# Performance work log

Hardware: AMD Instinct MI355X
Metric: run time of the kernel (lower is better)

Reference implementation:

```python
import jax, jax.numpy as jnp
import numpy as np

B, N = 128, 1024

def setup_inputs() -> dict:
    key = jax.random.key(0)
    k1, k2 = jax.random.split(key)
    probs = jax.random.uniform(k1, (B, N), dtype=jnp.float32)
    co_matrix = jax.random.uniform(k2, (N, N), dtype=jnp.float32)
    return {"probs": probs, "co_matrix": co_matrix}

def reference(probs, co_matrix):
    # diff[b, i, j] = probs[b, j] - probs[b, i]
    diff = probs[:, None, :] - probs[:, :, None]          # [B, N, N]
    weighted = jnp.square(diff) * co_matrix[None, :, :]   # [B, N, N]
    eps = 1e-8
    n_pos = jnp.sum((co_matrix > 0).astype(jnp.float32))
    # sum over (i, j) of mean over batch
    loss = jnp.sum(jnp.mean(weighted, axis=0)) / (n_pos + eps)
    return loss
```

## Files before the change

### kernel.cpp

```cpp
#include <hip/hip_runtime.h>


#define B_DIM 128
#define N_DIM 1024
#define TILE  64

__global__ __launch_bounds__(512) void tile_kernel(const float* __restrict__ P,
                                                   const float* __restrict__ C,
                                                   double* __restrict__ psum,
                                                   unsigned* __restrict__ pcnt) {
    __shared__ float Pi[B_DIM][TILE];
    __shared__ float Pj[B_DIM][TILE];
    __shared__ float ts[2 * TILE];
    __shared__ double wsum[8];
    __shared__ unsigned wcnt[8];

    const int tid = threadIdx.x;
    const int tj_blk = blockIdx.x & 15;
    const int ti_blk = blockIdx.x >> 4;
    const int i0 = ti_blk * TILE, j0 = tj_blk * TILE;

    const float4* P4 = (const float4*)P;
    float4* Pi4 = (float4*)&Pi[0][0];
    float4* Pj4 = (float4*)&Pj[0][0];
#pragma unroll
    for (int r = 0; r < 4; ++r) {
        int idx = r * 512 + tid;
        int b   = idx >> 4;
        int q   = idx & 15;
        Pi4[idx] = P4[b * (N_DIM / 4) + (i0 >> 2) + q];
        Pj4[idx] = P4[b * (N_DIM / 4) + (j0 >> 2) + q];
    }
    __syncthreads();

    if (tid < 2 * TILE) {
        const float* col = (tid < TILE) ? &Pi[0][tid] : &Pj[0][tid - TILE];
        float s = 0.f;
#pragma unroll 8
        for (int b = 0; b < B_DIM; ++b) {
            float v = col[b * TILE];
            s = fmaf(v, v, s);
        }
        ts[tid] = s;
    }
    __syncthreads();

    const int tx = tid & 15;
    const int ty = tid >> 4;
    float g00=0,g01=0,g02=0,g03=0, g10=0,g11=0,g12=0,g13=0;
#pragma unroll 8
    for (int b = 0; b < B_DIM; ++b) {
        float2 a = *(const float2*)&Pi[b][ty * 2];
        float4 c = *(const float4*)&Pj[b][tx * 4];
        g00 = fmaf(a.x, c.x, g00); g01 = fmaf(a.x, c.y, g01);
        g02 = fmaf(a.x, c.z, g02); g03 = fmaf(a.x, c.w, g03);
        g10 = fmaf(a.y, c.x, g10); g11 = fmaf(a.y, c.y, g11);
        g12 = fmaf(a.y, c.z, g12); g13 = fmaf(a.y, c.w, g13);
    }
    float gm[2][4] = {{g00,g01,g02,g03},{g10,g11,g12,g13}};

    float ti[2], tj[4];
#pragma unroll
    for (int r = 0; r < 2; ++r) ti[r] = ts[ty * 2 + r];
#pragma unroll
    for (int c = 0; c < 4; ++c) tj[c] = ts[TILE + tx * 4 + c];

    float acc = 0.f;
    unsigned cnt = 0;
    const float4* C4 = (const float4*)C;
#pragma unroll
    for (int r = 0; r < 2; ++r) {
        float4 cv = C4[(size_t)(i0 + ty * 2 + r) * (N_DIM / 4) + (j0 >> 2) + tx];
        acc = fmaf(cv.x, ti[r] + tj[0] - 2.f * gm[r][0], acc);
        acc = fmaf(cv.y, ti[r] + tj[1] - 2.f * gm[r][1], acc);
        acc = fmaf(cv.z, ti[r] + tj[2] - 2.f * gm[r][2], acc);
        acc = fmaf(cv.w, ti[r] + tj[3] - 2.f * gm[r][3], acc);
        cnt += (cv.x > 0.f) + (cv.y > 0.f) + (cv.z > 0.f) + (cv.w > 0.f);
    }

#pragma unroll
    for (int off = 32; off > 0; off >>= 1) {
        acc += __shfl_down(acc, off);
        cnt += __shfl_down(cnt, off);
    }
    const int wave = tid >> 6, lane = tid & 63;
    if (lane == 0) { wsum[wave] = (double)acc; wcnt[wave] = cnt; }
    __syncthreads();
    if (tid == 0) {
        double s = 0.0; unsigned c = 0;
#pragma unroll
        for (int w = 0; w < 8; ++w) { s += wsum[w]; c += wcnt[w]; }
        psum[blockIdx.x] = s;
        pcnt[blockIdx.x] = c;
    }
}

__global__ __launch_bounds__(256) void reduce_kernel(const double* __restrict__ psum,
                                                     const unsigned* __restrict__ pcnt,
                                                     float* __restrict__ out) {
    __shared__ double ws[4];
    __shared__ unsigned wc[4];
    const int tid = threadIdx.x;
    double s = psum[tid];
    unsigned c = pcnt[tid];
#pragma unroll
    for (int off = 32; off > 0; off >>= 1) {
        s += __shfl_down(s, off);
        c += __shfl_down(c, off);
    }
    const int wave = tid >> 6, lane = tid & 63;
    if (lane == 0) { ws[wave] = s; wc[wave] = c; }
    __syncthreads();
    if (tid == 0) {
        double st = ws[0] + ws[1] + ws[2] + ws[3];
        double ct = (double)(wc[0] + wc[1] + wc[2] + wc[3]);
        out[0] = (float)(st / ((double)B_DIM * (ct + 1e-8)));
    }
}

extern "C" void kernel_launch(void* const* d_in, const int* in_sizes, int n_in,
                              void* d_out, int out_size, void* d_ws, size_t ws_size,
                              hipStream_t stream) {
    const float* probs = (const float*)d_in[0];
    const float* co    = (const float*)d_in[1];
    float* out = (float*)d_out;

    double*   psum = (double*)d_ws;
    unsigned* pcnt = (unsigned*)((char*)d_ws + 256 * 8);

    tile_kernel<<<(N_DIM / TILE) * (N_DIM / TILE), 512, 0, stream>>>(probs, co, psum, pcnt);
    reduce_kernel<<<1, 256, 0, stream>>>(psum, pcnt, out);
}
```

Before: 65.99 us.

## Fuse into cooperative kernel with bf16 MFMA Gram computation

Replaces the two-kernel scheme with one cooperative kernel. Phase one transposes probs to bf16 and computes per-column sums of squares. After a grid sync, each block computes its 64x64 Gram tile with bf16 MFMA instructions and weights it by the co-matrix. A second grid sync lets block 0 do the final reduction. This removes the FP32 FMA inner loop and one kernel launch, at the cost of bf16 precision in the cross term (which risks cancellation error in ti+tj-2g) and two grid-wide barriers.

```diff
diff --git a/kernel.cpp b/kernel.cpp
--- a/kernel.cpp
+++ b/kernel.cpp
@@ -1,120 +1,119 @@
 #include <hip/hip_runtime.h>
+#include <hip/hip_cooperative_groups.h>
+
+namespace cg = cooperative_groups;
 
 
 #define B_DIM 128
 #define N_DIM 1024
-#define TILE  64
 
-__global__ __launch_bounds__(512) void tile_kernel(const float* __restrict__ P,
-                                                   const float* __restrict__ C,
-                                                   double* __restrict__ psum,
-                                                   unsigned* __restrict__ pcnt) {
-    __shared__ float Pi[B_DIM][TILE];
-    __shared__ float Pj[B_DIM][TILE];
-    __shared__ float ts[2 * TILE];
-    __shared__ double wsum[8];
-    __shared__ unsigned wcnt[8];
+typedef __bf16 bf16x8 __attribute__((ext_vector_type(8)));
+typedef float  f32x4  __attribute__((ext_vector_type(4)));
+typedef short  s16x8  __attribute__((ext_vector_type(8)));
 
-    const int tid = threadIdx.x;
-    const int tj_blk = blockIdx.x & 15;
-    const int ti_blk = blockIdx.x >> 4;
-    const int i0 = ti_blk * TILE, j0 = tj_blk * TILE;
+static __device__ inline unsigned short f2bf(float f) {
+    union { float f; unsigned u; } v; v.f = f;
+    unsigned r = (v.u + 0x7fffu + ((v.u >> 16) & 1u)) >> 16;
+    return (unsigned short)r;
+}
 
-    const float4* P4 = (const float4*)P;
-    float4* Pi4 = (float4*)&Pi[0][0];
-    float4* Pj4 = (float4*)&Pj[0][0];
+__global__ __launch_bounds__(256) void fused_kernel(const float* __restrict__ P,
+                                                    const float* __restrict__ C,
+                                                    float* __restrict__ out,
+                                                    unsigned short* __restrict__ PT,
+                                                    float* __restrict__ tws,
+                                                    float* __restrict__ psum,
+                                                    unsigned* __restrict__ pcnt) {
+    const int tid = threadIdx.x, bid = blockIdx.x;
+    const int l = tid & 63, w = tid >> 6;
+    __shared__ float    tp[4][4];
+    __shared__ float    wsum[4];
+    __shared__ unsigned wcnt[4];
+    __shared__ double   fsum[4];
+    __shared__ unsigned fcnt[4];
+
+    {
+        const int c = tid & 3, b = tid >> 2;
+        const int col = bid * 4 + c;
+        float p0 = P[b * N_DIM + col];
+        float p1 = P[(b + 64) * N_DIM + col];
+        PT[col * B_DIM + b]      = f2bf(p0);
+        PT[col * B_DIM + b + 64] = f2bf(p1);
+        float sq = fmaf(p0, p0, p1 * p1);
 #pragma unroll
-    for (int r = 0; r < 4; ++r) {
-        int idx = r * 512 + tid;
-        int b   = idx >> 4;
-        int q   = idx & 15;
-        Pi4[idx] = P4[b * (N_DIM / 4) + (i0 >> 2) + q];
-        Pj4[idx] = P4[b * (N_DIM / 4) + (j0 >> 2) + q];
+        for (int off = 4; off <= 32; off <<= 1) sq += __shfl_xor(sq, off);
+        if (l < 4) tp[w][l] = sq;
+        __syncthreads();
+        if (tid < 4) tws[bid * 4 + tid] = tp[0][tid] + tp[1][tid] + tp[2][tid] + tp[3][tid];
     }
-    __syncthreads();
+    __threadfence();
+    cg::this_grid().sync();
 
-    if (tid < 2 * TILE) {
-        const float* col = (tid < TILE) ? &Pi[0][tid] : &Pj[0][tid - TILE];
-        float s = 0.f;
-#pragma unroll 8
-        for (int b = 0; b < B_DIM; ++b) {
-            float v = col[b * TILE];
-            s = fmaf(v, v, s);
+    const int i0 = (bid >> 4) * 64, j0 = (bid & 15) * 64;
+    const s16x8* PT8 = (const s16x8*)PT;
+
+    bf16x8 A[4];
+    const int arow = i0 + w * 16 + (l & 15);
+#pragma unroll
+    for (int s = 0; s < 4; ++s) {
+        s16x8 raw = PT8[(arow * B_DIM + s * 32 + (l >> 4) * 8) >> 3];
+        A[s] = __builtin_bit_cast(bf16x8, raw);
+    }
+    float tr[4];
+#pragma unroll
+    for (int r = 0; r < 4; ++r) tr[r] = tws[i0 + w * 16 + (l >> 4) * 4 + r];
+
+    float loss = 0.f;
+    unsigned cnt = 0;
+#pragma unroll
+    for (int nt = 0; nt < 4; ++nt) {
+        const int bcol = j0 + nt * 16 + (l & 15);
+        f32x4 acc = {0.f, 0.f, 0.f, 0.f};
+#pragma unroll
+        for (int s = 0; s < 4; ++s) {
+            s16x8 raw = PT8[(bcol * B_DIM + s * 32 + (l >> 4) * 8) >> 3];
+            bf16x8 Bf = __builtin_bit_cast(bf16x8, raw);
+            acc = __builtin_amdgcn_mfma_f32_16x16x32_bf16(A[s], Bf, acc, 0, 0, 0);
         }
-        ts[tid] = s;
-    }
-    __syncthreads();
-
-    const int tx = tid & 15;
-    const int ty = tid >> 4;
-    float g00=0,g01=0,g02=0,g03=0, g10=0,g11=0,g12=0,g13=0;
-#pragma unroll 8
-    for (int b = 0; b < B_DIM; ++b) {
-        float2 a = *(const float2*)&Pi[b][ty * 2];
-        float4 c = *(const float4*)&Pj[b][tx * 4];
-        g00 = fmaf(a.x, c.x, g00); g01 = fmaf(a.x, c.y, g01);
-        g02 = fmaf(a.x, c.z, g02); g03 = fmaf(a.x, c.w, g03);
-        g10 = fmaf(a.y, c.x, g10); g11 = fmaf(a.y, c.y, g11);
-        g12 = fmaf(a.y, c.z, g12); g13 = fmaf(a.y, c.w, g13);
-    }
-    float gm[2][4] = {{g00,g01,g02,g03},{g10,g11,g12,g13}};
-
-    float ti[2], tj[4];
+        const float tc = tws[bcol];
 #pragma unroll
-    for (int r = 0; r < 2; ++r) ti[r] = ts[ty * 2 + r];
-#pragma unroll
-    for (int c = 0; c < 4; ++c) tj[c] = ts[TILE + tx * 4 + c];
-
-    float acc = 0.f;
-    unsigned cnt = 0;
-    const float4* C4 = (const float4*)C;
-#pragma unroll
-    for (int r = 0; r < 2; ++r) {
-        float4 cv = C4[(size_t)(i0 + ty * 2 + r) * (N_DIM / 4) + (j0 >> 2) + tx];
-        acc = fmaf(cv.x, ti[r] + tj[0] - 2.f * gm[r][0], acc);
-        acc = fmaf(cv.y, ti[r] + tj[1] - 2.f * gm[r][1], acc);
-        acc = fmaf(cv.z, ti[r] + tj[2] - 2.f * gm[r][2], acc);
-        acc = fmaf(cv.w, ti[r] + tj[3] - 2.f * gm[r][3], acc);
-        cnt += (cv.x > 0.f) + (cv.y > 0.f) + (cv.z > 0.f) + (cv.w > 0.f);
+        for (int r = 0; r < 4; ++r) {
+            const int gi = i0 + w * 16 + (l >> 4) * 4 + r;
+            float cv = C[gi * N_DIM + bcol];
+            loss = fmaf(cv, tr[r] + tc - 2.f * acc[r], loss);
+            cnt += (cv > 0.f) ? 1u : 0u;
+        }
     }
 
 #pragma unroll
     for (int off = 32; off > 0; off >>= 1) {
-        acc += __shfl_down(acc, off);
-        cnt += __shfl_down(cnt, off);
+        loss += __shfl_down(loss, off);
+        cnt  += __shfl_down(cnt, off);
     }
-    const int wave = tid >> 6, lane = tid & 63;
-    if (lane == 0) { wsum[wave] = (double)acc; wcnt[wave] = cnt; }
+    if (l == 0) { wsum[w] = loss; wcnt[w] = cnt; }
     __syncthreads();
     if (tid == 0) {
-        double s = 0.0; unsigned c = 0;
+        psum[bid] = wsum[0] + wsum[1] + wsum[2] + wsum[3];
+        pcnt[bid] = wcnt[0] + wcnt[1] + wcnt[2] + wcnt[3];
+    }
+    __threadfence();
+    cg::this_grid().sync();
+
+    if (bid == 0) {
+        double s = (double)psum[tid];
+        unsigned c = pcnt[tid];
 #pragma unroll
-        for (int w = 0; w < 8; ++w) { s += wsum[w]; c += wcnt[w]; }
-        psum[blockIdx.x] = s;
-        pcnt[blockIdx.x] = c;
-    }
-}
-
-__global__ __launch_bounds__(256) void reduce_kernel(const double* __restrict__ psum,
-                                                     const unsigned* __restrict__ pcnt,
-                                                     float* __restrict__ out) {
-    __shared__ double ws[4];
-    __shared__ unsigned wc[4];
-    const int tid = threadIdx.x;
-    double s = psum[tid];
-    unsigned c = pcnt[tid];
-#pragma unroll
-    for (int off = 32; off > 0; off >>= 1) {
-        s += __shfl_down(s, off);
-        c += __shfl_down(c, off);
-    }
-    const int wave = tid >> 6, lane = tid & 63;
-    if (lane == 0) { ws[wave] = s; wc[wave] = c; }
-    __syncthreads();
-    if (tid == 0) {
-        double st = ws[0] + ws[1] + ws[2] + ws[3];
-        double ct = (double)(wc[0] + wc[1] + wc[2] + wc[3]);
-        out[0] = (float)(st / ((double)B_DIM * (ct + 1e-8)));
+        for (int off = 32; off > 0; off >>= 1) {
+            s += __shfl_down(s, off);
+            c += __shfl_down(c, off);
+        }
+        if (l == 0) { fsum[w] = s; fcnt[w] = c; }
+        __syncthreads();
+        if (tid == 0) {
+            double st = fsum[0] + fsum[1] + fsum[2] + fsum[3];
+            double ct = (double)(fcnt[0] + fcnt[1] + fcnt[2] + fcnt[3]);
+            out[0] = (float)(st / ((double)B_DIM * (ct + 1e-8)));
+        }
     }
 }
 
@@ -125,9 +124,13 @@
     const float* co    = (const float*)d_in[1];
     float* out = (float*)d_out;
 
-    double*   psum = (double*)d_ws;
-    unsigned* pcnt = (unsigned*)((char*)d_ws + 256 * 8);
+    unsigned short* PT   = (unsigned short*)d_ws;
+    float*          tws  = (float*)((char*)d_ws + (256u << 10));
+    float*          psum = (float*)((char*)d_ws + (260u << 10));
+    unsigned*       pcnt = (unsigned*)((char*)d_ws + (261u << 10));
 
-    tile_kernel<<<(N_DIM / TILE) * (N_DIM / TILE), 512, 0, stream>>>(probs, co, psum, pcnt);
-    reduce_kernel<<<1, 256, 0, stream>>>(psum, pcnt, out);
+    void* args[] = {(void*)&probs, (void*)&co, (void*)&out,
+                    (void*)&PT, (void*)&tws, (void*)&psum, (void*)&pcnt};
+    hipLaunchCooperativeKernel((const void*)fused_kernel, dim3(256), dim3(256),
+                               args, 0, stream);
 }
```

After: 155.2 us. 2.35x slower.
